# Kernel optimization log

Measured on AMD Instinct MI355X. Metric: run time of the kernel, lower is better.

The kernel has to match this reference:

```python
import jax, jax.numpy as jnp
import numpy as np

NUM_HEADS = 16
DIM = 1280
HEAD_DIM = DIM // NUM_HEADS  # 80
N_TOKENS = 4096


def _rotate_half(x):
    x1, x2 = jnp.split(x, 2, axis=-1)
    return jnp.concatenate([-x2, x1], axis=-1)


def _apply_rotary_vision(t, freqs):
    # t: (N, H, D), freqs: (N, D//2)
    cos = jnp.tile(jnp.cos(freqs), (1, 2))[:, None, :]  # (N, 1, D)
    sin = jnp.tile(jnp.sin(freqs), (1, 2))[:, None, :]
    return t * cos + _rotate_half(t) * sin


def setup_inputs() -> dict:
    key = jax.random.key(0)
    ks = jax.random.split(key, 6)
    hidden_states = jax.random.normal(ks[0], (N_TOKENS, DIM), dtype=jnp.float32)
    # 4 packed variable-length image sequences
    cu_seqlens = jnp.array([0, 600, 1600, 2800, N_TOKENS], dtype=jnp.int32)
    rotary_pos_emb = jax.random.normal(ks[1], (N_TOKENS, HEAD_DIM // 2), dtype=jnp.float32)
    w_qkv = jax.random.normal(ks[2], (DIM, 3 * DIM), dtype=jnp.float32) * 0.02
    b_qkv = jax.random.normal(ks[3], (3 * DIM,), dtype=jnp.float32) * 0.02
    w_proj = jax.random.normal(ks[4], (DIM, DIM), dtype=jnp.float32) * 0.02
    b_proj = jax.random.normal(ks[5], (DIM,), dtype=jnp.float32) * 0.02
    return {"hidden_states": hidden_states, "cu_seqlens": cu_seqlens,
            "rotary_pos_emb": rotary_pos_emb, "w_qkv": w_qkv, "b_qkv": b_qkv,
            "w_proj": w_proj, "b_proj": b_proj}


def reference(hidden_states, cu_seqlens, rotary_pos_emb, w_qkv, b_qkv, w_proj, b_proj):
    N = hidden_states.shape[0]
    H, D = NUM_HEADS, HEAD_DIM
    qkv = hidden_states @ w_qkv + b_qkv                  # (N, 3*dim)
    qkv = qkv.reshape(N, 3, H, D)
    q, k, v = qkv[:, 0], qkv[:, 1], qkv[:, 2]            # (N, H, D)
    q = _apply_rotary_vision(q, rotary_pos_emb)
    k = _apply_rotary_vision(k, rotary_pos_emb)
    # segment id per token from cu_seqlens boundaries
    pos = jnp.arange(N, dtype=jnp.int32)
    seg = jnp.searchsorted(cu_seqlens, pos, side='right') - 1  # (N,)
    same_seg = seg[:, None] == seg[None, :]              # (N, N) bool
    scale = 1.0 / jnp.sqrt(jnp.asarray(D, dtype=q.dtype))
    scores = jnp.einsum('nhd,mhd->hnm', q, k) * scale    # (H, N, N)
    scores = jnp.where(same_seg[None, :, :], scores, jnp.finfo(scores.dtype).min)
    probs = jax.nn.softmax(scores, axis=-1)
    out = jnp.einsum('hnm,mhd->nhd', probs, v)           # (N, H, D)
    out = out.reshape(N, H * D)
    return out @ w_proj + b_proj
```

## Files before the change

kernel.cpp:

```cpp
#include <hip/hip_runtime.h>
#include <math.h>


#define N_TOK 4096
#define DIMM  1280
#define NHEAD 16
#define HD    80
#define QKVN  3840
#define KP    3840

typedef short bf16x8 __attribute__((ext_vector_type(8)));
typedef float f32x4  __attribute__((ext_vector_type(4)));

__device__ __forceinline__ unsigned short f2bf(float x) {
    unsigned int u = __float_as_uint(x);
    u += 0x7fff + ((u >> 16) & 1);
    return (unsigned short)(u >> 16);
}
__device__ __forceinline__ float bf2f(unsigned short h) {
    return __uint_as_float(((unsigned int)h) << 16);
}
__device__ __forceinline__ void gload_lds16(const void* g, void* l) {
    __builtin_amdgcn_global_load_lds(
        (const __attribute__((address_space(1))) unsigned int*)g,
        (__attribute__((address_space(3))) unsigned int*)l, 16, 0, 0);
}

#define MFMA16(a, b, c) __builtin_amdgcn_mfma_f32_16x16x32_bf16((a), (b), (c), 0, 0, 0)

__global__ void pack_A_kernel(const float* __restrict__ X, unsigned short* __restrict__ Ap)
{
    const int idx = blockIdx.x * blockDim.x + threadIdx.x;
    if (idx >= N_TOK * DIMM / 4) return;
    const int e = idx * 4;
    const int m = e / DIMM, k = e - (e / DIMM) * DIMM;
    const float4 v = *reinterpret_cast<const float4*>(&X[(size_t)m * DIMM + k]);
    ushort4 hi, lo;
    hi.x = f2bf(v.x); lo.x = f2bf(v.x - bf2f(hi.x));
    hi.y = f2bf(v.y); lo.y = f2bf(v.y - bf2f(hi.y));
    hi.z = f2bf(v.z); lo.z = f2bf(v.z - bf2f(hi.z));
    hi.w = f2bf(v.w); lo.w = f2bf(v.w - bf2f(hi.w));
    const size_t base = (size_t)m * KP + k;
    *reinterpret_cast<ushort4*>(&Ap[base])            = hi;
    *reinterpret_cast<ushort4*>(&Ap[base + DIMM])     = lo;
    *reinterpret_cast<ushort4*>(&Ap[base + 2 * DIMM]) = hi;
}

__global__ __launch_bounds__(256)
void pack_Bt_kernel(const float* __restrict__ W, unsigned short* __restrict__ Bt, int Ncols)
{
    __shared__ float Ts[32][33];
    const int k0 = blockIdx.x * 32, n0 = blockIdx.y * 32;
    const int t = threadIdx.x;
    const int r = t >> 3, c4 = (t & 7) * 4;
    const float4 v = *reinterpret_cast<const float4*>(&W[(size_t)(k0 + r) * Ncols + n0 + c4]);
    Ts[r][c4] = v.x; Ts[r][c4 + 1] = v.y; Ts[r][c4 + 2] = v.z; Ts[r][c4 + 3] = v.w;
    __syncthreads();
    float w0 = Ts[c4][r], w1 = Ts[c4 + 1][r], w2 = Ts[c4 + 2][r], w3 = Ts[c4 + 3][r];
    ushort4 hi, lo;
    hi.x = f2bf(w0); lo.x = f2bf(w0 - bf2f(hi.x));
    hi.y = f2bf(w1); lo.y = f2bf(w1 - bf2f(hi.y));
    hi.z = f2bf(w2); lo.z = f2bf(w2 - bf2f(hi.z));
    hi.w = f2bf(w3); lo.w = f2bf(w3 - bf2f(hi.w));
    const size_t base = (size_t)(n0 + r) * KP + k0 + c4;
    *reinterpret_cast<ushort4*>(&Bt[base])            = hi;
    *reinterpret_cast<ushort4*>(&Bt[base + DIMM])     = hi;
    *reinterpret_cast<ushort4*>(&Bt[base + 2 * DIMM]) = lo;
}

template<int EPI>
__global__ __launch_bounds__(256)
void gemm_mfma(const unsigned short* __restrict__ A, const unsigned short* __restrict__ Bt,
               const float* __restrict__ bias, float* __restrict__ out, int Ncols, int nwg)
{
    __shared__ unsigned short As[128 * 32];
    __shared__ unsigned short Bs[128 * 32];

    const int tid  = threadIdx.x;
    const int w    = tid >> 6, lane = tid & 63;

    const int lin = blockIdx.x;
    const int wg  = (lin & 7) * (nwg >> 3) + (lin >> 3);
    const int m0  = (wg & 31) * 128;
    const int n0  = (wg >> 5) * 128;

    const int wm   = w >> 1, wn = w & 1;
    const int lm   = lane & 15, kb = lane >> 4;

    const char* Ag = (const char*)(A  + (size_t)(m0 + w * 32 + (lane >> 2)) * KP) + (lane & 3) * 16;
    const char* Bg = (const char*)(Bt + (size_t)(n0 + w * 32 + (lane >> 2)) * KP) + (lane & 3) * 16;
    char* AsB = (char*)As + w * 2048;
    char* BsB = (char*)Bs + w * 2048;
    const size_t rowskip = (size_t)16 * KP * 2;

    f32x4 acc[4][4] = {};

    for (int k0 = 0; k0 < KP; k0 += 32) {
        const size_t kb2 = (size_t)k0 * 2;
        gload_lds16(Ag + kb2,           AsB);
        gload_lds16(Ag + kb2 + rowskip, AsB + 1024);
        gload_lds16(Bg + kb2,           BsB);
        gload_lds16(Bg + kb2 + rowskip, BsB + 1024);
        __syncthreads();

        bf16x8 a[4], b[4];
        #pragma unroll
        for (int mf = 0; mf < 4; ++mf)
            a[mf] = *reinterpret_cast<const bf16x8*>(&As[(wm * 64 + mf * 16 + lm) * 32 + kb * 8]);
        #pragma unroll
        for (int nf = 0; nf < 4; ++nf)
            b[nf] = *reinterpret_cast<const bf16x8*>(&Bs[(wn * 64 + nf * 16 + lm) * 32 + kb * 8]);
        #pragma unroll
        for (int mf = 0; mf < 4; ++mf)
            #pragma unroll
            for (int nf = 0; nf < 4; ++nf)
                acc[mf][nf] = MFMA16(a[mf], b[nf], acc[mf][nf]);
        __syncthreads();
    }

    #pragma unroll
    for (int nf = 0; nf < 4; ++nf) {
        const int col = n0 + wn * 64 + nf * 16 + lm;
        const float bb = bias[col];
        #pragma unroll
        for (int mf = 0; mf < 4; ++mf) {
            #pragma unroll
            for (int r = 0; r < 4; ++r) {
                const int row = m0 + wm * 64 + mf * 16 + kb * 4 + r;
                const float c = acc[mf][nf][r] + bb;
                if (EPI == 0) {
                    out[(size_t)row * Ncols + col] = c;
                } else {
                    const int part = col / DIMM;
                    const int rem  = col - part * DIMM;
                    const int hh   = rem / HD;
                    const int d    = rem - hh * HD;
                    out[(((size_t)(part * NHEAD + hh)) * N_TOK + row) * HD + d] = c;
                }
            }
        }
    }
}

__global__ void rope_kernel(const float* __restrict__ freqs, float* __restrict__ q,
                            const float* __restrict__ k, unsigned short* __restrict__ Kp)
{
    const int idx = blockIdx.x * blockDim.x + threadIdx.x;
    if (idx >= N_TOK * NHEAD * 40) return;
    const int dp = idx % 40;
    const int t  = idx / 40;
    const int h  = t & 15;
    const int n  = t >> 4;

    const float f = freqs[n * 40 + dp];
    const float c = cosf(f);
    const float s = sinf(f);

    const size_t base = ((size_t)h * N_TOK + n) * HD;
    const float q1 = q[base + dp], q2 = q[base + dp + 40];
    q[base + dp]      = q1 * c - q2 * s;
    q[base + dp + 40] = q2 * c + q1 * s;

    const float scale = 0.11180339887498949f;
    const float k1 = k[base + dp], k2 = k[base + dp + 40];
    const float kr1 = (k1 * c - k2 * s) * scale;
    const float kr2 = (k2 * c + k1 * s) * scale;

    const size_t hi = ((size_t)(h * 2) * N_TOK + n) * 104;
    const size_t lo = ((size_t)(h * 2 + 1) * N_TOK + n) * 104;
    const unsigned short h1 = f2bf(kr1);
    Kp[hi + dp]      = h1;
    Kp[lo + dp]      = f2bf(kr1 - bf2f(h1));
    const unsigned short h2 = f2bf(kr2);
    Kp[hi + dp + 40] = h2;
    Kp[lo + dp + 40] = f2bf(kr2 - bf2f(h2));
    if (dp < 12) {
        Kp[hi + 80 + dp] = 0; Kp[hi + 92 + dp] = 0;
        Kp[lo + 80 + dp] = 0; Kp[lo + 92 + dp] = 0;
    }
}

__global__ __launch_bounds__(256)
void vpack_kernel(const float* __restrict__ v, unsigned short* __restrict__ Vt)
{
    __shared__ float T[32][81];
    const int t = blockIdx.x, h = blockIdx.y;
    const int kt = t * 32;
    for (int e = threadIdx.x; e < 32 * 80; e += 256) {
        const int key = e / 80, d = e - (e / 80) * 80;
        T[key][d] = v[((size_t)h * N_TOK + kt + key) * HD + d];
    }
    __syncthreads();
    unsigned short* base = Vt + ((size_t)h * 128 + t) * 6400;
    for (int e = threadIdx.x; e < 3200; e += 256) {
        const int d = e / 40, key = e - (e / 40) * 40;
        const float x = (key < 32) ? T[key][d] : 0.f;
        const unsigned short hi = f2bf(x);
        base[e]        = hi;
        base[3200 + e] = f2bf(x - bf2f(hi));
    }
}

__global__ __launch_bounds__(512)
void attn_mfma(const float* __restrict__ qbuf, const unsigned short* __restrict__ Kp,
               const unsigned short* __restrict__ Vt, const int* __restrict__ cu,
               unsigned short* __restrict__ Ap)
{
    __shared__ __align__(16) unsigned short KhS[2][3328];
    __shared__ __align__(16) unsigned short KlS[2][3328];
    __shared__ __align__(16) unsigned short VS [2][6400];
    __shared__ __align__(16) unsigned short Pw [8][640];

    const int tid  = threadIdx.x;
    const int w    = tid >> 6, lane = tid & 63;
    const int lm   = lane & 15, g = lane >> 4;

    const int lin = blockIdx.x;
    const int h   = (lin & 7) * 2 + ((lin >> 3) & 1);
    const int q0  = (lin >> 4) * 128;

    const int c1 = cu[1], c2 = cu[2], c3 = cu[3];
    #define SEGOF(n) ((int)((n) >= c1) + (int)((n) >= c2) + (int)((n) >= c3))
    const int seg_first = SEGOF(q0);
    const int seg_last  = SEGOF(q0 + 127);
    const int cuv[5] = {0, c1, c2, c3, N_TOK};
    const int kmin = cuv[seg_first], kmax = cuv[seg_last + 1];
    const int kt0 = kmin & ~31;
    const int ntiles = (kmax - kt0 + 31) >> 5;

    const size_t hb = (size_t)h * N_TOK;

    bf16x8 qh[3], ql[3];
    const int qrow = q0 + w * 16 + lm;
    {
        const float* qp = qbuf + (hb + qrow) * HD;
        #pragma unroll
        for (int ks = 0; ks < 3; ++ks) {
            #pragma unroll
            for (int j = 0; j < 8; ++j) {
                const int d = ks * 32 + g * 8 + j;
                const float x = (d < HD) ? qp[d] : 0.f;
                const unsigned short hi = f2bf(x);
                qh[ks][j] = (short)hi;
                ql[ks][j] = (short)f2bf(x - bf2f(hi));
            }
        }
    }
    const int sq  = SEGOF(qrow);
    const int klo = cuv[sq], khi = cuv[sq + 1];

    float mrow = -1e30f, lrow = 0.f;
    f32x4 accO[5] = {};

    auto issue = [&](int buf, int kt) {
        const char* sK  = (const char*)(Kp + ((size_t)(h * 2)     * N_TOK + kt) * 104);
        const char* sKl = (const char*)(Kp + ((size_t)(h * 2 + 1) * N_TOK + kt) * 104);
        const char* sV  = (const char*)(Vt + ((size_t)h * 128 + (kt >> 5)) * 6400);
        char* dK  = (char*)&KhS[buf][0];
        char* dKl = (char*)&KlS[buf][0];
        char* dV  = (char*)&VS[buf][0];
        for (int j = w; j < 27; j += 8) {
            const char* s; char* d; int off; int half;
            if (j < 7)       { s = sK;  d = dK;  off = j * 1024;        half = (j == 6); }
            else if (j < 14) { s = sKl; d = dKl; off = (j - 7) * 1024;  half = (j == 13); }
            else             { s = sV;  d = dV;  off = (j - 14) * 1024; half = (j == 26); }
            if (!half || lane < 32)
                gload_lds16(s + off + (size_t)lane * 16, d + off);
        }
    };

    issue(0, kt0);
    __syncthreads();

    for (int ti = 0; ti < ntiles; ++ti) {
        const int kt  = kt0 + ti * 32;
        const int buf = ti & 1;
        if (ti + 1 < ntiles) issue(buf ^ 1, kt + 32);

        const unsigned short* Kh = &KhS[buf][0];
        const unsigned short* Kl = &KlS[buf][0];
        const unsigned short* Vb = &VS[buf][0];

        f32x4 s0 = {0.f, 0.f, 0.f, 0.f}, s1 = {0.f, 0.f, 0.f, 0.f};
        #pragma unroll
        for (int ks = 0; ks < 3; ++ks) {
            const bf16x8 k0h = *reinterpret_cast<const bf16x8*>(&Kh[lm * 104 + ks * 32 + g * 8]);
            const bf16x8 k0l = *reinterpret_cast<const bf16x8*>(&Kl[lm * 104 + ks * 32 + g * 8]);
            const bf16x8 k1h = *reinterpret_cast<const bf16x8*>(&Kh[(16 + lm) * 104 + ks * 32 + g * 8]);
            const bf16x8 k1l = *reinterpret_cast<const bf16x8*>(&Kl[(16 + lm) * 104 + ks * 32 + g * 8]);
            s0 = MFMA16(k0h, qh[ks], s0);
            s0 = MFMA16(k0h, ql[ks], s0);
            s0 = MFMA16(k0l, qh[ks], s0);
            s1 = MFMA16(k1h, qh[ks], s1);
            s1 = MFMA16(k1h, ql[ks], s1);
            s1 = MFMA16(k1l, qh[ks], s1);
        }

        bool v0m[4], v1m[4];
        #pragma unroll
        for (int r = 0; r < 4; ++r) {
            const int j0 = kt + g * 4 + r;
            const int j1 = j0 + 16;
            v0m[r] = (j0 >= klo) && (j0 < khi);
            v1m[r] = (j1 >= klo) && (j1 < khi);
        }

        float tm = -1e30f;
        #pragma unroll
        for (int r = 0; r < 4; ++r) {
            tm = fmaxf(tm, fmaxf(v0m[r] ? s0[r] : -1e30f, v1m[r] ? s1[r] : -1e30f));
        }
        tm = fmaxf(tm, __shfl_xor(tm, 16));
        tm = fmaxf(tm, __shfl_xor(tm, 32));

        const bool defer = __all(tm <= mrow + 8.0f);
        if (!defer) {
            const float mn = fmaxf(mrow, tm);
            const float sc = __expf(mrow - mn);
            mrow = mn;
            lrow *= sc;
            float scq[4];
            #pragma unroll
            for (int r = 0; r < 4; ++r) scq[r] = __shfl(sc, ((lane >> 4) << 2) + r);
            #pragma unroll
            for (int f = 0; f < 5; ++f) {
                accO[f][0] *= scq[0]; accO[f][1] *= scq[1];
                accO[f][2] *= scq[2]; accO[f][3] *= scq[3];
            }
        }

        float p0[4], p1[4], rs = 0.f;
        #pragma unroll
        for (int r = 0; r < 4; ++r) {
            p0[r] = v0m[r] ? __expf(s0[r] - mrow) : 0.f;
            p1[r] = v1m[r] ? __expf(s1[r] - mrow) : 0.f;
            rs += p0[r] + p1[r];
        }
        rs += __shfl_xor(rs, 16);
        rs += __shfl_xor(rs, 32);
        lrow += rs;

        {
            unsigned int u;
            u = (unsigned int)f2bf(p0[0]) | ((unsigned int)f2bf(p0[1]) << 16);
            *reinterpret_cast<unsigned int*>(&Pw[w][lm * 40 + g * 4])      = u;
            u = (unsigned int)f2bf(p0[2]) | ((unsigned int)f2bf(p0[3]) << 16);
            *reinterpret_cast<unsigned int*>(&Pw[w][lm * 40 + g * 4 + 2])  = u;
            u = (unsigned int)f2bf(p1[0]) | ((unsigned int)f2bf(p1[1]) << 16);
            *reinterpret_cast<unsigned int*>(&Pw[w][lm * 40 + 16 + g * 4]) = u;
            u = (unsigned int)f2bf(p1[2]) | ((unsigned int)f2bf(p1[3]) << 16);
            *reinterpret_cast<unsigned int*>(&Pw[w][lm * 40 + 18 + g * 4]) = u;
        }
        asm volatile("s_waitcnt lgkmcnt(0)" ::: "memory");
        __builtin_amdgcn_sched_barrier(0);

        const bf16x8 pa = *reinterpret_cast<const bf16x8*>(&Pw[w][lm * 40 + g * 8]);
        #pragma unroll
        for (int f = 0; f < 5; ++f) {
            const bf16x8 vh = *reinterpret_cast<const bf16x8*>(&Vb[(f * 16 + lm) * 40 + g * 8]);
            const bf16x8 vl = *reinterpret_cast<const bf16x8*>(&Vb[3200 + (f * 16 + lm) * 40 + g * 8]);
            accO[f] = MFMA16(pa, vh, accO[f]);
            accO[f] = MFMA16(pa, vl, accO[f]);
        }

        __syncthreads();
    }

    const float linv = 1.f / lrow;
    float invq[4];
    #pragma unroll
    for (int r = 0; r < 4; ++r) invq[r] = __shfl(linv, ((lane >> 4) << 2) + r);

    #pragma unroll
    for (int r = 0; r < 4; ++r) {
        const int n = q0 + w * 16 + g * 4 + r;
        const size_t rb = (size_t)n * KP + h * HD;
        #pragma unroll
        for (int f = 0; f < 5; ++f) {
            const float v = accO[f][r] * invq[r];
            const unsigned short hi = f2bf(v);
            const unsigned short lo = f2bf(v - bf2f(hi));
            Ap[rb + f * 16 + lm]            = hi;
            Ap[rb + DIMM + f * 16 + lm]     = lo;
            Ap[rb + 2 * DIMM + f * 16 + lm] = hi;
        }
    }
    #undef SEGOF
}

extern "C" void kernel_launch(void* const* d_in, const int* in_sizes, int n_in,
                              void* d_out, int out_size, void* d_ws, size_t ws_size,
                              hipStream_t stream)
{
    const float* hidden = (const float*)d_in[0];
    const int*   cu     = (const int*)  d_in[1];
    const float* rope   = (const float*)d_in[2];
    const float* w_qkv  = (const float*)d_in[3];
    const float* b_qkv  = (const float*)d_in[4];
    const float* w_proj = (const float*)d_in[5];
    const float* b_proj = (const float*)d_in[6];
    float*       out    = (float*)d_out;

    const size_t perbuf = (size_t)NHEAD * N_TOK * HD;
    float* qbuf = (float*)d_ws;
    float* kbuf = qbuf + perbuf;
    float* vbuf = kbuf + perbuf;
    unsigned short* Apack = (unsigned short*)(vbuf + perbuf);
    unsigned short* BtQ   = Apack + (size_t)N_TOK * KP;
    unsigned short* BtP   = BtQ + (size_t)QKVN * KP;
    unsigned short* Vt    = BtP + (size_t)DIMM * KP;
    unsigned short* Kp    = BtQ;

    pack_A_kernel<<<(N_TOK * DIMM / 4 + 255) / 256, 256, 0, stream>>>(hidden, Apack);
    pack_Bt_kernel<<<dim3(DIMM / 32, QKVN / 32), 256, 0, stream>>>(w_qkv, BtQ, QKVN);
    pack_Bt_kernel<<<dim3(DIMM / 32, DIMM / 32), 256, 0, stream>>>(w_proj, BtP, DIMM);

    gemm_mfma<1><<<960, 256, 0, stream>>>(Apack, BtQ, b_qkv, qbuf, QKVN, 960);

    rope_kernel<<<(N_TOK * NHEAD * 40 + 255) / 256, 256, 0, stream>>>(rope, qbuf, kbuf, Kp);
    vpack_kernel<<<dim3(128, NHEAD), 256, 0, stream>>>(vbuf, Vt);

    attn_mfma<<<512, 512, 0, stream>>>(qbuf, Kp, Vt, cu, Apack);

    gemm_mfma<0><<<320, 256, 0, stream>>>(Apack, BtP, b_proj, out, DIMM, 320);
}
```

Before: 564.6 us.

## Retile K/V packing, deepen attention prefetch, keep P in registers, remap GEMM tiles

K is now packed into per-32-key tiles with hi and lo halves adjacent, so each tile loads contiguously into one LDS buffer. The attention loop prefetches two tiles ahead and waits with vmcnt counts plus raw barriers instead of a full __syncthreads per tile. V columns are permuted during packing so the P fragment can be built directly in registers, which removes the per-wave LDS round trip for P. GEMM workgroup-to-tile mapping is changed to a fixed XCD-aware layout. The risks are that the hand-counted vmcnt waits are fragile, and the launch_bounds occupancy hint of 4 may force register spills.

```diff
diff --git a/kernel.cpp b/kernel.cpp
--- a/kernel.cpp
+++ b/kernel.cpp
@@ -71,7 +71,7 @@
 template<int EPI>
 __global__ __launch_bounds__(256)
 void gemm_mfma(const unsigned short* __restrict__ A, const unsigned short* __restrict__ Bt,
-               const float* __restrict__ bias, float* __restrict__ out, int Ncols, int nwg)
+               const float* __restrict__ bias, float* __restrict__ out, int Ncols)
 {
     __shared__ unsigned short As[128 * 32];
     __shared__ unsigned short Bs[128 * 32];
@@ -80,9 +80,16 @@
     const int w    = tid >> 6, lane = tid & 63;
 
     const int lin = blockIdx.x;
-    const int wg  = (lin & 7) * (nwg >> 3) + (lin >> 3);
-    const int m0  = (wg & 31) * 128;
-    const int n0  = (wg >> 5) * 128;
+    const int x   = lin & 7;
+    const int l   = lin >> 3;
+    int m0, n0;
+    if (EPI == 1) {
+        m0 = ((x >> 1) * 8 + (l & 7)) * 128;
+        n0 = ((x & 1) * 15 + (l >> 3)) * 128;
+    } else {
+        m0 = (x * 4 + (l & 3)) * 128;
+        n0 = (l >> 2) * 128;
+    }
 
     const int wm   = w >> 1, wn = w & 1;
     const int lm   = lane & 15, kb = lane >> 4;
@@ -143,7 +150,7 @@
 }
 
 __global__ void rope_kernel(const float* __restrict__ freqs, float* __restrict__ q,
-                            const float* __restrict__ k, unsigned short* __restrict__ Kp)
+                            const float* __restrict__ k, unsigned short* __restrict__ Kpk)
 {
     const int idx = blockIdx.x * blockDim.x + threadIdx.x;
     if (idx >= N_TOK * NHEAD * 40) return;
@@ -166,17 +173,18 @@
     const float kr1 = (k1 * c - k2 * s) * scale;
     const float kr2 = (k2 * c + k1 * s) * scale;
 
-    const size_t hi = ((size_t)(h * 2) * N_TOK + n) * 104;
-    const size_t lo = ((size_t)(h * 2 + 1) * N_TOK + n) * 104;
+    const int tile = n >> 5, r = n & 31;
+    const size_t hi = ((size_t)(h * 128 + tile) * 2 + 0) * 3328 + r * 104;
+    const size_t lo = ((size_t)(h * 128 + tile) * 2 + 1) * 3328 + r * 104;
     const unsigned short h1 = f2bf(kr1);
-    Kp[hi + dp]      = h1;
-    Kp[lo + dp]      = f2bf(kr1 - bf2f(h1));
+    Kpk[hi + dp]      = h1;
+    Kpk[lo + dp]      = f2bf(kr1 - bf2f(h1));
     const unsigned short h2 = f2bf(kr2);
-    Kp[hi + dp + 40] = h2;
-    Kp[lo + dp + 40] = f2bf(kr2 - bf2f(h2));
+    Kpk[hi + dp + 40] = h2;
+    Kpk[lo + dp + 40] = f2bf(kr2 - bf2f(h2));
     if (dp < 12) {
-        Kp[hi + 80 + dp] = 0; Kp[hi + 92 + dp] = 0;
-        Kp[lo + 80 + dp] = 0; Kp[lo + 92 + dp] = 0;
+        Kpk[hi + 80 + dp] = 0; Kpk[hi + 92 + dp] = 0;
+        Kpk[lo + 80 + dp] = 0; Kpk[lo + 92 + dp] = 0;
     }
 }
 
@@ -193,23 +201,25 @@
     __syncthreads();
     unsigned short* base = Vt + ((size_t)h * 128 + t) * 6400;
     for (int e = threadIdx.x; e < 3200; e += 256) {
-        const int d = e / 40, key = e - (e / 40) * 40;
-        const float x = (key < 32) ? T[key][d] : 0.f;
+        const int d = e / 40, col = e - (e / 40) * 40;
+        float x = 0.f;
+        if (col < 32) {
+            const int key = (((col & 7) < 4) ? 0 : 16) + 4 * (col >> 3) + (col & 3);
+            x = T[key][d];
+        }
         const unsigned short hi = f2bf(x);
         base[e]        = hi;
         base[3200 + e] = f2bf(x - bf2f(hi));
     }
 }
 
-__global__ __launch_bounds__(512)
-void attn_mfma(const float* __restrict__ qbuf, const unsigned short* __restrict__ Kp,
+__global__ __launch_bounds__(512, 4)
+void attn_mfma(const float* __restrict__ qbuf, const unsigned short* __restrict__ Kpk,
                const unsigned short* __restrict__ Vt, const int* __restrict__ cu,
                unsigned short* __restrict__ Ap)
 {
-    __shared__ __align__(16) unsigned short KhS[2][3328];
-    __shared__ __align__(16) unsigned short KlS[2][3328];
-    __shared__ __align__(16) unsigned short VS [2][6400];
-    __shared__ __align__(16) unsigned short Pw [8][640];
+    __shared__ __align__(16) unsigned short KS[2][6656];
+    __shared__ __align__(16) unsigned short VS[2][6400];
 
     const int tid  = threadIdx.x;
     const int w    = tid >> 6, lane = tid & 63;
@@ -226,6 +236,7 @@
     const int cuv[5] = {0, c1, c2, c3, N_TOK};
     const int kmin = cuv[seg_first], kmax = cuv[seg_last + 1];
     const int kt0 = kmin & ~31;
+    const int t0  = kt0 >> 5;
     const int ntiles = (kmax - kt0 + 31) >> 5;
 
     const size_t hb = (size_t)h * N_TOK;
@@ -252,42 +263,48 @@
     float mrow = -1e30f, lrow = 0.f;
     f32x4 accO[5] = {};
 
-    auto issue = [&](int buf, int kt) {
-        const char* sK  = (const char*)(Kp + ((size_t)(h * 2)     * N_TOK + kt) * 104);
-        const char* sKl = (const char*)(Kp + ((size_t)(h * 2 + 1) * N_TOK + kt) * 104);
-        const char* sV  = (const char*)(Vt + ((size_t)h * 128 + (kt >> 5)) * 6400);
-        char* dK  = (char*)&KhS[buf][0];
-        char* dKl = (char*)&KlS[buf][0];
-        char* dV  = (char*)&VS[buf][0];
-        for (int j = w; j < 27; j += 8) {
-            const char* s; char* d; int off; int half;
-            if (j < 7)       { s = sK;  d = dK;  off = j * 1024;        half = (j == 6); }
-            else if (j < 14) { s = sKl; d = dKl; off = (j - 7) * 1024;  half = (j == 13); }
-            else             { s = sV;  d = dV;  off = (j - 14) * 1024; half = (j == 26); }
-            if (!half || lane < 32)
-                gload_lds16(s + off + (size_t)lane * 16, d + off);
+    auto issue = [&](int buf, int tg) {
+        const char* sK = (const char*)(Kpk + ((size_t)(h * 128 + tg) * 2) * 3328);
+        const char* sV = (const char*)(Vt  +  (size_t)(h * 128 + tg) * 6400);
+        char* dK = (char*)&KS[buf][0];
+        char* dV = (char*)&VS[buf][0];
+        for (int j = w; j < 26; j += 8) {
+            if (j < 13) {
+                gload_lds16(sK + j * 1024 + (size_t)lane * 16, dK + j * 1024);
+            } else if (j < 25) {
+                gload_lds16(sV + (j - 13) * 1024 + (size_t)lane * 16, dV + (j - 13) * 1024);
+            } else if (lane < 32) {
+                gload_lds16(sV + 12288 + (size_t)lane * 16, dV + 12288);
+            }
         }
     };
 
-    issue(0, kt0);
-    __syncthreads();
+    issue(0, t0);
+    if (ntiles > 1) issue(1, t0 + 1);
 
     for (int ti = 0; ti < ntiles; ++ti) {
+        const int buf = ti & 1;
         const int kt  = kt0 + ti * 32;
-        const int buf = ti & 1;
-        if (ti + 1 < ntiles) issue(buf ^ 1, kt + 32);
-
-        const unsigned short* Kh = &KhS[buf][0];
-        const unsigned short* Kl = &KlS[buf][0];
+
+        if (ti + 1 < ntiles) {
+            if (w < 2) asm volatile("s_waitcnt vmcnt(4)" ::: "memory");
+            else       asm volatile("s_waitcnt vmcnt(3)" ::: "memory");
+        } else {
+            asm volatile("s_waitcnt vmcnt(0)" ::: "memory");
+        }
+        __builtin_amdgcn_s_barrier();
+        asm volatile("" ::: "memory");
+
+        const unsigned short* Kb = &KS[buf][0];
         const unsigned short* Vb = &VS[buf][0];
 
         f32x4 s0 = {0.f, 0.f, 0.f, 0.f}, s1 = {0.f, 0.f, 0.f, 0.f};
         #pragma unroll
         for (int ks = 0; ks < 3; ++ks) {
-            const bf16x8 k0h = *reinterpret_cast<const bf16x8*>(&Kh[lm * 104 + ks * 32 + g * 8]);
-            const bf16x8 k0l = *reinterpret_cast<const bf16x8*>(&Kl[lm * 104 + ks * 32 + g * 8]);
-            const bf16x8 k1h = *reinterpret_cast<const bf16x8*>(&Kh[(16 + lm) * 104 + ks * 32 + g * 8]);
-            const bf16x8 k1l = *reinterpret_cast<const bf16x8*>(&Kl[(16 + lm) * 104 + ks * 32 + g * 8]);
+            const bf16x8 k0h = *reinterpret_cast<const bf16x8*>(&Kb[lm * 104 + ks * 32 + g * 8]);
+            const bf16x8 k0l = *reinterpret_cast<const bf16x8*>(&Kb[3328 + lm * 104 + ks * 32 + g * 8]);
+            const bf16x8 k1h = *reinterpret_cast<const bf16x8*>(&Kb[(16 + lm) * 104 + ks * 32 + g * 8]);
+            const bf16x8 k1l = *reinterpret_cast<const bf16x8*>(&Kb[3328 + (16 + lm) * 104 + ks * 32 + g * 8]);
             s0 = MFMA16(k0h, qh[ks], s0);
             s0 = MFMA16(k0h, ql[ks], s0);
             s0 = MFMA16(k0l, qh[ks], s0);
@@ -307,9 +324,8 @@
 
         float tm = -1e30f;
         #pragma unroll
-        for (int r = 0; r < 4; ++r) {
+        for (int r = 0; r < 4; ++r)
             tm = fmaxf(tm, fmaxf(v0m[r] ? s0[r] : -1e30f, v1m[r] ? s1[r] : -1e30f));
-        }
         tm = fmaxf(tm, __shfl_xor(tm, 16));
         tm = fmaxf(tm, __shfl_xor(tm, 32));
 
@@ -340,21 +356,12 @@
         rs += __shfl_xor(rs, 32);
         lrow += rs;
 
-        {
-            unsigned int u;
-            u = (unsigned int)f2bf(p0[0]) | ((unsigned int)f2bf(p0[1]) << 16);
-            *reinterpret_cast<unsigned int*>(&Pw[w][lm * 40 + g * 4])      = u;
-            u = (unsigned int)f2bf(p0[2]) | ((unsigned int)f2bf(p0[3]) << 16);
-            *reinterpret_cast<unsigned int*>(&Pw[w][lm * 40 + g * 4 + 2])  = u;
-            u = (unsigned int)f2bf(p1[0]) | ((unsigned int)f2bf(p1[1]) << 16);
-            *reinterpret_cast<unsigned int*>(&Pw[w][lm * 40 + 16 + g * 4]) = u;
-            u = (unsigned int)f2bf(p1[2]) | ((unsigned int)f2bf(p1[3]) << 16);
-            *reinterpret_cast<unsigned int*>(&Pw[w][lm * 40 + 18 + g * 4]) = u;
-        }
-        asm volatile("s_waitcnt lgkmcnt(0)" ::: "memory");
-        __builtin_amdgcn_sched_barrier(0);
-
-        const bf16x8 pa = *reinterpret_cast<const bf16x8*>(&Pw[w][lm * 40 + g * 8]);
+        bf16x8 pa;
+        pa[0] = (short)f2bf(p0[0]); pa[1] = (short)f2bf(p0[1]);
+        pa[2] = (short)f2bf(p0[2]); pa[3] = (short)f2bf(p0[3]);
+        pa[4] = (short)f2bf(p1[0]); pa[5] = (short)f2bf(p1[1]);
+        pa[6] = (short)f2bf(p1[2]); pa[7] = (short)f2bf(p1[3]);
+
         #pragma unroll
         for (int f = 0; f < 5; ++f) {
             const bf16x8 vh = *reinterpret_cast<const bf16x8*>(&Vb[(f * 16 + lm) * 40 + g * 8]);
@@ -363,7 +370,10 @@
             accO[f] = MFMA16(pa, vl, accO[f]);
         }
 
-        __syncthreads();
+        asm volatile("s_waitcnt lgkmcnt(0)" ::: "memory");
+        __builtin_amdgcn_s_barrier();
+        asm volatile("" ::: "memory");
+        if (ti + 2 < ntiles) issue(buf, t0 + ti + 2);
     }
 
     const float linv = 1.f / lrow;
@@ -409,18 +419,18 @@
     unsigned short* BtQ   = Apack + (size_t)N_TOK * KP;
     unsigned short* BtP   = BtQ + (size_t)QKVN * KP;
     unsigned short* Vt    = BtP + (size_t)DIMM * KP;
-    unsigned short* Kp    = BtQ;
+    unsigned short* Kpk   = BtQ;
 
     pack_A_kernel<<<(N_TOK * DIMM / 4 + 255) / 256, 256, 0, stream>>>(hidden, Apack);
     pack_Bt_kernel<<<dim3(DIMM / 32, QKVN / 32), 256, 0, stream>>>(w_qkv, BtQ, QKVN);
     pack_Bt_kernel<<<dim3(DIMM / 32, DIMM / 32), 256, 0, stream>>>(w_proj, BtP, DIMM);
 
-    gemm_mfma<1><<<960, 256, 0, stream>>>(Apack, BtQ, b_qkv, qbuf, QKVN, 960);
-
-    rope_kernel<<<(N_TOK * NHEAD * 40 + 255) / 256, 256, 0, stream>>>(rope, qbuf, kbuf, Kp);
+    gemm_mfma<1><<<960, 256, 0, stream>>>(Apack, BtQ, b_qkv, qbuf, QKVN);
+
+    rope_kernel<<<(N_TOK * NHEAD * 40 + 255) / 256, 256, 0, stream>>>(rope, qbuf, kbuf, Kpk);
     vpack_kernel<<<dim3(128, NHEAD), 256, 0, stream>>>(vbuf, Vt);
 
-    attn_mfma<<<512, 512, 0, stream>>>(qbuf, Kp, Vt, cu, Apack);
-
-    gemm_mfma<0><<<320, 256, 0, stream>>>(Apack, BtP, b_proj, out, DIMM, 320);
-}
+    attn_mfma<<<512, 512, 0, stream>>>(qbuf, Kpk, Vt, cu, Apack);
+
+    gemm_mfma<0><<<320, 256, 0, stream>>>(Apack, BtP, b_proj, out, DIMM);
+}
```

Measured after the change: 548.9 us. 1.03x faster.
